# Optimization experiments

Hardware: AMD Instinct MI355X
Metric: run time of the kernel (lower is better)

The kernel has to match this reference:

```python
import jax, jax.numpy as jnp
import numpy as np
import math

EPS = 1e-5  # BatchNorm eps; eval mode with running_mean=0, running_var=1


def maxpool(x, k, p):
    return jax.lax.reduce_window(x, -jnp.inf, jax.lax.max,
                                 (1, 1, k, k), (1, 1, 1, 1),
                                 ((0, 0), (0, 0), (p, p), (p, p)))


def conv1x1(x, w, b=None):
    # x: [B,Cin,H,W], w: [Cout,Cin]
    y = jnp.einsum('oi,bihw->bohw', w, x)
    if b is not None:
        y = y + b[None, :, None, None]
    return y


def bn_eval(x, g, b):
    scale = g / jnp.sqrt(1.0 + EPS)
    return x * scale[None, :, None, None] + b[None, :, None, None]


def setup_inputs() -> dict:
    B, C, H, W = 2, 64, 80, 80
    c1, c2, c3 = 21, 21, 22
    ch = 32  # C//2
    ks = jax.random.split(jax.random.key(0), 16)
    s = 0.05
    inp = {
        'x': jax.random.normal(ks[0], (B, C, H, W), jnp.float32),
        'q1_w': jax.random.normal(ks[1], (c1, c1), jnp.float32) * s,
        'q1_g': jnp.ones((c1,), jnp.float32),
        'q1_b': jnp.zeros((c1,), jnp.float32),
        'q2_w': jax.random.normal(ks[2], (c2, c2), jnp.float32) * s,
        'q2_g': jnp.ones((c2,), jnp.float32),
        'q2_b': jnp.zeros((c2,), jnp.float32),
        'q3_w': jax.random.normal(ks[3], (c3, c3), jnp.float32) * s,
        'q3_g': jnp.ones((c3,), jnp.float32),
        'q3_b': jnp.zeros((c3,), jnp.float32),
        'k_hf_w': jax.random.normal(ks[4], (ch, C), jnp.float32) * s,
        'k_hf_b': jnp.zeros((ch,), jnp.float32),
        'k_lf_w': jax.random.normal(ks[5], (C - ch, C), jnp.float32) * s,
        'k_lf_b': jnp.zeros((C - ch,), jnp.float32),
        'k_fuse_w': jax.random.normal(ks[6], (C, C), jnp.float32) * s,
        'k_fuse_b': jnp.zeros((C,), jnp.float32),
        'v_bn_g': jnp.ones((C,), jnp.float32),
        'v_bn_b': jnp.zeros((C,), jnp.float32),
        'v_w': jax.random.normal(ks[7], (C, C), jnp.float32) * s,
        'v_b': jnp.zeros((C,), jnp.float32),
        'out_w': jax.random.normal(ks[8], (C, C), jnp.float32) * s,
        'out_b': jnp.zeros((C,), jnp.float32),
    }
    return inp


def reference(x, q1_w, q1_g, q1_b, q2_w, q2_g, q2_b, q3_w, q3_g, q3_b,
              k_hf_w, k_hf_b, k_lf_w, k_lf_b, k_fuse_w, k_fuse_b,
              v_bn_g, v_bn_b, v_w, v_b, out_w, out_b):
    B, C, H, W = x.shape
    N = H * W
    c1 = q1_w.shape[0]
    c2 = q2_w.shape[0]
    # Q: ThreeGroupConvQ (split -> 1x1 conv (no bias) -> BN -> ReLU -> concat)
    x1, x2, x3 = jnp.split(x, [c1, c1 + c2], axis=1)
    y1 = jax.nn.relu(bn_eval(conv1x1(x1, q1_w), q1_g, q1_b))
    y2 = jax.nn.relu(bn_eval(conv1x1(x2, q2_w), q2_g, q2_b))
    y3 = jax.nn.relu(bn_eval(conv1x1(x3, q3_w), q3_g, q3_b))
    Q = jnp.concatenate([y1, y2, y3], axis=1)
    # K: ThermalStructureExtractor
    p3 = maxpool(x, 3, 1)
    p5 = maxpool(x, 5, 2)
    low = (p3 + p5) * 0.5
    high = conv1x1(x - low, k_hf_w, k_hf_b)
    lowp = conv1x1(low, k_lf_w, k_lf_b)
    K = conv1x1(jnp.concatenate([high, lowp], axis=1), k_fuse_w, k_fuse_b)
    # V: BN -> 1x1 conv
    V = conv1x1(bn_eval(x, v_bn_g, v_bn_b), v_w, v_b)
    # attention over N = H*W spatial tokens, channel features
    Qc = Q.reshape(B, C, N)
    Kc = K.reshape(B, C, N)
    Vc = V.reshape(B, C, N)
    attn = jax.nn.softmax(
        jnp.einsum('bcn,bcm->bnm', Qc, Kc) / math.sqrt(C), axis=-1)  # [B,N,N]
    out = jnp.einsum('bnm,bcm->bcn', attn, Vc).reshape(B, C, H, W)
    return conv1x1(out, out_w, out_b) + x
```

## Files before the change

### kernel.cpp

```cpp
#include <hip/hip_runtime.h>
#include <hip/hip_bf16.h>


#define BATCH 2
#define CH 64
#define HH 80
#define WW 80
#define NN 6400
#define NT 100
#define KS 5
#define KTPS (NT/KS)
#define EPSV 1e-5f
#define NEGBIG (-1e30f)
#define LOG2E8 0.18033688f

typedef __hip_bfloat16 bf16;
typedef __attribute__((ext_vector_type(8))) short short8;
typedef __attribute__((ext_vector_type(4))) float f4;
#define MFMA16 __builtin_amdgcn_mfma_f32_16x16x32_bf16

__device__ __forceinline__ float b2f(bf16 v){ return __bfloat162float(v); }
__device__ __forceinline__ bf16 f2b(float v){ return __float2bfloat16(v); }
__device__ __forceinline__ ushort f2bu(float v){ return ((__hip_bfloat16_raw)__float2bfloat16(v)).x; }
__device__ __forceinline__ float bu2f(ushort u){
  union { unsigned int i; float f; } w; w.i = ((unsigned int)u) << 16; return w.f;
}
__device__ __forceinline__ unsigned pkbf(float a, float b){
  union { __hip_bfloat162 h2; unsigned u; } cv;
  cv.h2 = __float22bfloat162_rn(make_float2(a, b));
  return cv.u;
}
__device__ __forceinline__ float fexp2(float x){
#if __has_builtin(__builtin_amdgcn_exp2f)
  return __builtin_amdgcn_exp2f(x);
#else
  return exp2f(x);
#endif
}
__device__ __forceinline__ int swz(int row, int colb){
  return row*128 + (colb ^ ((row & 7) << 4));
}
__device__ __forceinline__ void sync_lds_only(){
  asm volatile("s_waitcnt lgkmcnt(0)" ::: "memory");
  __builtin_amdgcn_s_barrier();
  __builtin_amdgcn_sched_barrier(0);
  asm volatile("" ::: "memory");
}

#define OFF_BIAS 0
#define OFF_WH_B 768
#define OFF_LOW_B (768 + 32768)
#define OFF_Q_B   (OFF_LOW_B + BATCH*CH*NN*2)
#define OFF_K_B   (OFF_Q_B   + BATCH*CH*NN*2)
#define OFF_V_B   (OFF_K_B   + BATCH*CH*NN*2)
#define OFF_P_B   (OFF_V_B   + BATCH*CH*NN*2)
#define OFF_ML_B  (OFF_P_B   + BATCH*NT*KS*4096*2)

__global__ __launch_bounds__(256) void setup_fold(
    const float* __restrict__ q1w, const float* __restrict__ q1g, const float* __restrict__ q1b,
    const float* __restrict__ q2w, const float* __restrict__ q2g, const float* __restrict__ q2b,
    const float* __restrict__ q3w, const float* __restrict__ q3g, const float* __restrict__ q3b,
    const float* __restrict__ khw, const float* __restrict__ khb,
    const float* __restrict__ klw, const float* __restrict__ klb,
    const float* __restrict__ kfw, const float* __restrict__ kfb,
    const float* __restrict__ vg,  const float* __restrict__ vbnb,
    const float* __restrict__ vw,  const float* __restrict__ vb,
    const float* __restrict__ outw,
    float* __restrict__ biasf, bf16* __restrict__ wh)
{
  __shared__ __align__(16) float skf[4096];
  __shared__ __align__(16) float skh[2048];
  __shared__ __align__(16) float skl[2048];
  __shared__ __align__(16) float sow[4096];
  __shared__ __align__(16) float svw[4096];
  __shared__ float sbv[64];

  int tid = threadIdx.x;
  int blk = blockIdx.x;
  #pragma unroll
  for (int i = 0; i < 4; ++i) {
    *(float4*)&skf[(i*256 + tid)*4] = *(const float4*)&kfw[(i*256 + tid)*4];
    *(float4*)&sow[(i*256 + tid)*4] = *(const float4*)&outw[(i*256 + tid)*4];
    *(float4*)&svw[(i*256 + tid)*4] = *(const float4*)&vw[(i*256 + tid)*4];
  }
  #pragma unroll
  for (int i = 0; i < 2; ++i) {
    *(float4*)&skh[(i*256 + tid)*4] = *(const float4*)&khw[(i*256 + tid)*4];
    *(float4*)&skl[(i*256 + tid)*4] = *(const float4*)&klw[(i*256 + tid)*4];
  }
  __syncthreads();

  float rs = rsqrtf(1.0f + EPSV);
  if (tid < 64) {
    int j = tid;
    float bvo = vb[j];
    for (int ci2 = 0; ci2 < 64; ++ci2) bvo += svw[j*64 + ci2] * vbnb[ci2];
    sbv[j] = bvo;
  }

  bf16* wq   = wh;
  bf16* wvp  = wh + 4096;
  bf16* wa1  = wh + 8192;
  bf16* wa2m = wh + 12288;

  int t = blk*256 + tid;
  int ci = t & 63, co = t >> 6;
  int o = co*64 + ci;

  float w = 0.f, g;
  if (co < 21)      { g = q1g[co];    w = (ci < 21)              ? q1w[co*21 + ci]            : 0.f; }
  else if (co < 42) { g = q2g[co-21]; w = (ci >= 21 && ci < 42)  ? q2w[(co-21)*21 + (ci-21)]  : 0.f; }
  else              { g = q3g[co-42]; w = (ci >= 42)             ? q3w[(co-42)*22 + (ci-42)]  : 0.f; }
  wq[o] = f2b(w * g * rs * LOG2E8);

  float a1 = 0.f, a2 = 0.f;
  #pragma unroll
  for (int j = 0; j < 32; ++j) {
    a1 += skf[co*64 + j]      * skh[j*64 + ci];
    a2 += skf[co*64 + 32 + j] * skl[j*64 + ci];
  }
  wa1[o]  = f2b(a1);
  wa2m[o] = f2b(a2 - a1);

  float av = 0.f;
  #pragma unroll
  for (int j = 0; j < 64; ++j)
    av += sow[co*64 + j] * svw[j*64 + ci];
  wvp[o] = f2b(av * vg[ci] * rs);

  if (blk == 0 && tid < 64) {
    int c2 = tid;
    float bq;
    if (c2 < 21)      bq = q1b[c2];
    else if (c2 < 42) bq = q2b[c2-21];
    else              bq = q3b[c2-42];
    biasf[c2] = bq * LOG2E8;
    float bk = kfb[c2];
    #pragma unroll
    for (int j = 0; j < 32; ++j) {
      bk += skf[c2*64 + j]      * khb[j];
      bk += skf[c2*64 + 32 + j] * klb[j];
    }
    biasf[64 + c2] = bk;
    float bvp = 0.f;
    #pragma unroll
    for (int j = 0; j < 64; ++j) bvp += sow[c2*64 + j] * sbv[j];
    biasf[128 + c2] = bvp;
  }
}

__global__ __launch_bounds__(256) void pool_low(const float* __restrict__ x,
                                                bf16* __restrict__ lowg)
{
  int t4 = (blockIdx.x*256 + threadIdx.x)*4;
  int bc = t4 / NN; int n = t4 % NN;
  int h = n / WW, w0 = n % WW;
  const float* p = x + bc*NN;
  float m5[4], m3[4];
  #pragma unroll
  for (int j=0;j<4;++j){ m5[j]=NEGBIG; m3[j]=NEGBIG; }
  #pragma unroll
  for (int dh = -2; dh <= 2; ++dh) {
    int hh = h + dh; if (hh < 0 || hh >= HH) continue;
    float r[12];
    const float* row = p + hh*WW;
    if (w0 >= 4)      { float4 a = *(const float4*)&row[w0-4]; r[0]=a.x;r[1]=a.y;r[2]=a.z;r[3]=a.w; }
    else              { r[0]=NEGBIG;r[1]=NEGBIG;r[2]=NEGBIG;r[3]=NEGBIG; }
    { float4 a = *(const float4*)&row[w0]; r[4]=a.x;r[5]=a.y;r[6]=a.z;r[7]=a.w; }
    if (w0 + 7 < WW)  { float4 a = *(const float4*)&row[w0+4]; r[8]=a.x;r[9]=a.y;r[10]=a.z;r[11]=a.w; }
    else              { r[8]=NEGBIG;r[9]=NEGBIG;r[10]=NEGBIG;r[11]=NEGBIG; }
    bool in3 = (dh >= -1 && dh <= 1);
    #pragma unroll
    for (int j=0;j<4;++j) {
      float v3 = fmaxf(fmaxf(r[3+j], r[4+j]), r[5+j]);
      float v5 = fmaxf(fmaxf(r[2+j], v3), r[6+j]);
      m5[j] = fmaxf(m5[j], v5);
      if (in3) m3[j] = fmaxf(m3[j], v3);
    }
  }
  ushort4 o;
  o.x = f2bu(0.5f*(m3[0]+m5[0]));
  o.y = f2bu(0.5f*(m3[1]+m5[1]));
  o.z = f2bu(0.5f*(m3[2]+m5[2]));
  o.w = f2bu(0.5f*(m3[3]+m5[3]));
  *(ushort4*)&lowg[t4] = o;
}

__global__ __launch_bounds__(256, 2) void qkv_kernel(
    const float* __restrict__ x, const float* __restrict__ biasf,
    const bf16* __restrict__ wh, const bf16* __restrict__ lowg,
    bf16* __restrict__ qgT, bf16* __restrict__ kgT, bf16* __restrict__ vgc)
{
  __shared__ __align__(16) char xT[8192];
  __shared__ __align__(16) char lT[8192];
  __shared__ float bias[192];

  int tid = threadIdx.x;
  int blk = blockIdx.x;
  int b = blk / NT, tile = blk % NT;
  int n0 = tile*64;
  int wv = tid >> 6, lane = tid & 63, ln = lane & 15, quad = lane >> 4;

  if (tid < 192) bias[tid] = biasf[tid];

  {
    int cq = tid & 15, nq = tid >> 4;
    const float* xp = x + (size_t)(b*CH + cq*4)*NN + n0 + nq*4;
    float4 x0 = *(const float4*)&xp[0*NN];
    float4 x1 = *(const float4*)&xp[(size_t)1*NN];
    float4 x2 = *(const float4*)&xp[(size_t)2*NN];
    float4 x3 = *(const float4*)&xp[(size_t)3*NN];
    const bf16* lp = lowg + (size_t)(b*CH + cq*4)*NN + n0 + nq*4;
    uint2 l0 = *(const uint2*)&lp[0*NN];
    uint2 l1 = *(const uint2*)&lp[(size_t)1*NN];
    uint2 l2 = *(const uint2*)&lp[(size_t)2*NN];
    uint2 l3 = *(const uint2*)&lp[(size_t)3*NN];
    uint2 w;
    w.x = pkbf(x0.x, x1.x); w.y = pkbf(x2.x, x3.x);
    *(uint2*)(xT + swz(nq*4+0, cq*8)) = w;
    w.x = (l0.x & 0xffffu) | ((l1.x & 0xffffu) << 16);
    w.y = (l2.x & 0xffffu) | ((l3.x & 0xffffu) << 16);
    *(uint2*)(lT + swz(nq*4+0, cq*8)) = w;
    w.x = pkbf(x0.y, x1.y); w.y = pkbf(x2.y, x3.y);
    *(uint2*)(xT + swz(nq*4+1, cq*8)) = w;
    w.x = (l0.x >> 16) | ((l1.x >> 16) << 16);
    w.y = (l2.x >> 16) | ((l3.x >> 16) << 16);
    *(uint2*)(lT + swz(nq*4+1, cq*8)) = w;
    w.x = pkbf(x0.z, x1.z); w.y = pkbf(x2.z, x3.z);
    *(uint2*)(xT + swz(nq*4+2, cq*8)) = w;
    w.x = (l0.y & 0xffffu) | ((l1.y & 0xffffu) << 16);
    w.y = (l2.y & 0xffffu) | ((l3.y & 0xffffu) << 16);
    *(uint2*)(lT + swz(nq*4+2, cq*8)) = w;
    w.x = pkbf(x0.w, x1.w); w.y = pkbf(x2.w, x3.w);
    *(uint2*)(xT + swz(nq*4+3, cq*8)) = w;
    w.x = (l0.y >> 16) | ((l1.y >> 16) << 16);
    w.y = (l2.y >> 16) | ((l3.y >> 16) << 16);
    *(uint2*)(lT + swz(nq*4+3, cq*8)) = w;
  }
  __syncthreads();

  short8 xb00 = *(const short8*)(xT + swz(0*16 + ln, quad*16));
  short8 xb01 = *(const short8*)(xT + swz(0*16 + ln, 64 + quad*16));
  short8 xb10 = *(const short8*)(xT + swz(1*16 + ln, quad*16));
  short8 xb11 = *(const short8*)(xT + swz(1*16 + ln, 64 + quad*16));
  short8 xb20 = *(const short8*)(xT + swz(2*16 + ln, quad*16));
  short8 xb21 = *(const short8*)(xT + swz(2*16 + ln, 64 + quad*16));
  short8 xb30 = *(const short8*)(xT + swz(3*16 + ln, quad*16));
  short8 xb31 = *(const short8*)(xT + swz(3*16 + ln, 64 + quad*16));
  short8 xa0 = *(const short8*)(xT + swz(wv*16 + ln, quad*16));
  short8 xa1 = *(const short8*)(xT + swz(wv*16 + ln, 64 + quad*16));

  int cb = wv*16 + quad*4;
  const bf16* wqp  = wh;
  const bf16* wvpp = wh + 4096;
  const bf16* wa1p = wh + 8192;
  const bf16* wa2p = wh + 12288;
  int wrow = (wv*16 + ln)*64;

  {
    {
      short8 w0 = *(const short8*)&wvpp[(0*16 + ln)*64 + quad*8];
      short8 w1 = *(const short8*)&wvpp[(0*16 + ln)*64 + 32 + quad*8];
      float bv = bias[128 + 0*16 + ln];
      f4 a = (f4){bv, bv, bv, bv};
      a = MFMA16(xa0, w0, a, 0, 0, 0);
      a = MFMA16(xa1, w1, a, 0, 0, 0);
      uint2 pk; pk.x = pkbf(a[0], a[1]); pk.y = pkbf(a[2], a[3]);
      *(uint2*)&vgc[(size_t)(b*CH + 0*16 + ln)*NN + n0 + cb] = pk;
    }
    {
      short8 w0 = *(const short8*)&wvpp[(1*16 + ln)*64 + quad*8];
      short8 w1 = *(const short8*)&wvpp[(1*16 + ln)*64 + 32 + quad*8];
      float bv = bias[128 + 1*16 + ln];
      f4 a = (f4){bv, bv, bv, bv};
      a = MFMA16(xa0, w0, a, 0, 0, 0);
      a = MFMA16(xa1, w1, a, 0, 0, 0);
      uint2 pk; pk.x = pkbf(a[0], a[1]); pk.y = pkbf(a[2], a[3]);
      *(uint2*)&vgc[(size_t)(b*CH + 1*16 + ln)*NN + n0 + cb] = pk;
    }
    {
      short8 w0 = *(const short8*)&wvpp[(2*16 + ln)*64 + quad*8];
      short8 w1 = *(const short8*)&wvpp[(2*16 + ln)*64 + 32 + quad*8];
      float bv = bias[128 + 2*16 + ln];
      f4 a = (f4){bv, bv, bv, bv};
      a = MFMA16(xa0, w0, a, 0, 0, 0);
      a = MFMA16(xa1, w1, a, 0, 0, 0);
      uint2 pk; pk.x = pkbf(a[0], a[1]); pk.y = pkbf(a[2], a[3]);
      *(uint2*)&vgc[(size_t)(b*CH + 2*16 + ln)*NN + n0 + cb] = pk;
    }
    {
      short8 w0 = *(const short8*)&wvpp[(3*16 + ln)*64 + quad*8];
      short8 w1 = *(const short8*)&wvpp[(3*16 + ln)*64 + 32 + quad*8];
      float bv = bias[128 + 3*16 + ln];
      f4 a = (f4){bv, bv, bv, bv};
      a = MFMA16(xa0, w0, a, 0, 0, 0);
      a = MFMA16(xa1, w1, a, 0, 0, 0);
      uint2 pk; pk.x = pkbf(a[0], a[1]); pk.y = pkbf(a[2], a[3]);
      *(uint2*)&vgc[(size_t)(b*CH + 3*16 + ln)*NN + n0 + cb] = pk;
    }
  }

  {
    short8 wq0 = *(const short8*)&wqp[wrow + quad*8];
    short8 wq1 = *(const short8*)&wqp[wrow + 32 + quad*8];
    f4 bQ;
    bQ[0] = bias[cb+0]; bQ[1] = bias[cb+1]; bQ[2] = bias[cb+2]; bQ[3] = bias[cb+3];
    {
      f4 a = bQ;
      a = MFMA16(wq0, xb00, a, 0, 0, 0);
      a = MFMA16(wq1, xb01, a, 0, 0, 0);
      uint2 pk;
      pk.x = pkbf(fmaxf(a[0],0.f), fmaxf(a[1],0.f));
      pk.y = pkbf(fmaxf(a[2],0.f), fmaxf(a[3],0.f));
      *(uint2*)&qgT[(size_t)(b*NN + n0 + 0*16 + ln)*64 + cb] = pk;
    }
    {
      f4 a = bQ;
      a = MFMA16(wq0, xb10, a, 0, 0, 0);
      a = MFMA16(wq1, xb11, a, 0, 0, 0);
      uint2 pk;
      pk.x = pkbf(fmaxf(a[0],0.f), fmaxf(a[1],0.f));
      pk.y = pkbf(fmaxf(a[2],0.f), fmaxf(a[3],0.f));
      *(uint2*)&qgT[(size_t)(b*NN + n0 + 1*16 + ln)*64 + cb] = pk;
    }
    {
      f4 a = bQ;
      a = MFMA16(wq0, xb20, a, 0, 0, 0);
      a = MFMA16(wq1, xb21, a, 0, 0, 0);
      uint2 pk;
      pk.x = pkbf(fmaxf(a[0],0.f), fmaxf(a[1],0.f));
      pk.y = pkbf(fmaxf(a[2],0.f), fmaxf(a[3],0.f));
      *(uint2*)&qgT[(size_t)(b*NN + n0 + 2*16 + ln)*64 + cb] = pk;
    }
    {
      f4 a = bQ;
      a = MFMA16(wq0, xb30, a, 0, 0, 0);
      a = MFMA16(wq1, xb31, a, 0, 0, 0);
      uint2 pk;
      pk.x = pkbf(fmaxf(a[0],0.f), fmaxf(a[1],0.f));
      pk.y = pkbf(fmaxf(a[2],0.f), fmaxf(a[3],0.f));
      *(uint2*)&qgT[(size_t)(b*NN + n0 + 3*16 + ln)*64 + cb] = pk;
    }
  }

  {
    short8 wa10 = *(const short8*)&wa1p[wrow + quad*8];
    short8 wa11 = *(const short8*)&wa1p[wrow + 32 + quad*8];
    short8 wm0  = *(const short8*)&wa2p[wrow + quad*8];
    short8 wm1  = *(const short8*)&wa2p[wrow + 32 + quad*8];
    short8 lb00 = *(const short8*)(lT + swz(0*16 + ln, quad*16));
    short8 lb01 = *(const short8*)(lT + swz(0*16 + ln, 64 + quad*16));
    short8 lb10 = *(const short8*)(lT + swz(1*16 + ln, quad*16));
    short8 lb11 = *(const short8*)(lT + swz(1*16 + ln, 64 + quad*16));
    short8 lb20 = *(const short8*)(lT + swz(2*16 + ln, quad*16));
    short8 lb21 = *(const short8*)(lT + swz(2*16 + ln, 64 + quad*16));
    short8 lb30 = *(const short8*)(lT + swz(3*16 + ln, quad*16));
    short8 lb31 = *(const short8*)(lT + swz(3*16 + ln, 64 + quad*16));
    f4 bK;
    bK[0] = bias[64+cb+0]; bK[1] = bias[64+cb+1];
    bK[2] = bias[64+cb+2]; bK[3] = bias[64+cb+3];
    {
      f4 a = bK;
      a = MFMA16(wa10, xb00, a, 0, 0, 0);
      a = MFMA16(wa11, xb01, a, 0, 0, 0);
      a = MFMA16(wm0,  lb00, a, 0, 0, 0);
      a = MFMA16(wm1,  lb01, a, 0, 0, 0);
      uint2 pk; pk.x = pkbf(a[0], a[1]); pk.y = pkbf(a[2], a[3]);
      *(uint2*)&kgT[(size_t)(b*NN + n0 + 0*16 + ln)*64 + cb] = pk;
    }
    {
      f4 a = bK;
      a = MFMA16(wa10, xb10, a, 0, 0, 0);
      a = MFMA16(wa11, xb11, a, 0, 0, 0);
      a = MFMA16(wm0,  lb10, a, 0, 0, 0);
      a = MFMA16(wm1,  lb11, a, 0, 0, 0);
      uint2 pk; pk.x = pkbf(a[0], a[1]); pk.y = pkbf(a[2], a[3]);
      *(uint2*)&kgT[(size_t)(b*NN + n0 + 1*16 + ln)*64 + cb] = pk;
    }
    {
      f4 a = bK;
      a = MFMA16(wa10, xb20, a, 0, 0, 0);
      a = MFMA16(wa11, xb21, a, 0, 0, 0);
      a = MFMA16(wm0,  lb20, a, 0, 0, 0);
      a = MFMA16(wm1,  lb21, a, 0, 0, 0);
      uint2 pk; pk.x = pkbf(a[0], a[1]); pk.y = pkbf(a[2], a[3]);
      *(uint2*)&kgT[(size_t)(b*NN + n0 + 2*16 + ln)*64 + cb] = pk;
    }
    {
      f4 a = bK;
      a = MFMA16(wa10, xb30, a, 0, 0, 0);
      a = MFMA16(wa11, xb31, a, 0, 0, 0);
      a = MFMA16(wm0,  lb30, a, 0, 0, 0);
      a = MFMA16(wm1,  lb31, a, 0, 0, 0);
      uint2 pk; pk.x = pkbf(a[0], a[1]); pk.y = pkbf(a[2], a[3]);
      *(uint2*)&kgT[(size_t)(b*NN + n0 + 3*16 + ln)*64 + cb] = pk;
    }
  }
}

__global__ __launch_bounds__(256, 2) void attn_partial(
    const bf16* __restrict__ qgT, const bf16* __restrict__ kgT, const bf16* __restrict__ vgc,
    ushort* __restrict__ part, float* __restrict__ pml)
{
  __shared__ __align__(16) char smem[32768];
  __shared__ float lred[256];

  int tid = threadIdx.x;
  int blk = blockIdx.x;
  int b = blk / (NT*KS);
  int rem = blk % (NT*KS);
  int tile = rem / KS, split = rem % KS;
  int n0 = tile*64;
  int wv = tid >> 6, lane = tid & 63, ln = lane & 15, quad = lane >> 4;
  int mbase = split*KTPS*64;

  int r0 = tid >> 3,         c0 = (tid & 7)*8;
  int r1 = 32 + (tid >> 3),  c1 = (tid & 7)*8;

  {
    uint4 qa = *(const uint4*)&qgT[(size_t)(b*NN + n0 + r0)*64 + c0];
    uint4 qb = *(const uint4*)&qgT[(size_t)(b*NN + n0 + r1)*64 + c1];
    *(uint4*)(smem + swz(r0, c0*2)) = qa;
    *(uint4*)(smem + swz(r1, c1*2)) = qb;
  }
  __syncthreads();
  short8 bq00 = *(const short8*)(smem + swz( 0*16 + ln, quad*16));
  short8 bq01 = *(const short8*)(smem + swz( 0*16 + ln, 64 + quad*16));
  short8 bq10 = *(const short8*)(smem + swz( 1*16 + ln, quad*16));
  short8 bq11 = *(const short8*)(smem + swz( 1*16 + ln, 64 + quad*16));
  short8 bq20 = *(const short8*)(smem + swz( 2*16 + ln, quad*16));
  short8 bq21 = *(const short8*)(smem + swz( 2*16 + ln, 64 + quad*16));
  short8 bq30 = *(const short8*)(smem + swz( 3*16 + ln, quad*16));
  short8 bq31 = *(const short8*)(smem + swz( 3*16 + ln, 64 + quad*16));
  {
    uint4 va  = *(const uint4*)&vgc[(size_t)(b*CH + r0)*NN + mbase + c0];
    uint4 vb4 = *(const uint4*)&vgc[(size_t)(b*CH + r1)*NN + mbase + c1];
    *(uint4*)(smem + 16384 + swz(r0, c0*2)) = va;
    *(uint4*)(smem + 16384 + swz(r1, c1*2)) = vb4;
  }
  const bf16* kb = kgT + (size_t)(b*NN + mbase + wv*16 + ln)*64;
  short8 ak0 = *(const short8*)&kb[quad*8];
  short8 ak1 = *(const short8*)&kb[32 + quad*8];
  __syncthreads();

  f4 accO0 = (f4){0.f,0.f,0.f,0.f};
  f4 accO1 = (f4){0.f,0.f,0.f,0.f};
  f4 accO2 = (f4){0.f,0.f,0.f,0.f};
  f4 accO3 = (f4){0.f,0.f,0.f,0.f};
  float lacc0 = 0.f, lacc1 = 0.f, lacc2 = 0.f, lacc3 = 0.f;

  uint4 vr0, vr1;
  short8 an0, an1;
  for (int kt = 0; kt < KTPS; ++kt) {
    const int po = (kt & 1) * 8192;
    const int vo = 16384 + (kt & 1) * 8192;
    {
      int ktn = (kt + 1 < KTPS) ? kt + 1 : kt;
      int m1 = mbase + ktn*64;
      vr0 = *(const uint4*)&vgc[(size_t)(b*CH + r0)*NN + m1 + c0];
      vr1 = *(const uint4*)&vgc[(size_t)(b*CH + r1)*NN + m1 + c1];
      an0 = *(const short8*)&kb[(size_t)ktn*4096 + quad*8];
      an1 = *(const short8*)&kb[(size_t)ktn*4096 + 32 + quad*8];
    }

    f4 accS0, accS1, accS2, accS3;
    {
      f4 z = (f4){0.f,0.f,0.f,0.f};
      z = MFMA16(ak0, bq00, z, 0, 0, 0);
      accS0 = MFMA16(ak1, bq01, z, 0, 0, 0);
    }
    {
      f4 z = (f4){0.f,0.f,0.f,0.f};
      z = MFMA16(ak0, bq10, z, 0, 0, 0);
      accS1 = MFMA16(ak1, bq11, z, 0, 0, 0);
    }
    {
      f4 z = (f4){0.f,0.f,0.f,0.f};
      z = MFMA16(ak0, bq20, z, 0, 0, 0);
      accS2 = MFMA16(ak1, bq21, z, 0, 0, 0);
    }
    {
      f4 z = (f4){0.f,0.f,0.f,0.f};
      z = MFMA16(ak0, bq30, z, 0, 0, 0);
      accS3 = MFMA16(ak1, bq31, z, 0, 0, 0);
    }
    {
      float p0 = fexp2(accS0[0]), p1 = fexp2(accS0[1]);
      float p2 = fexp2(accS0[2]), p3 = fexp2(accS0[3]);
      lacc0 += (p0 + p1) + (p2 + p3);
      uint2 pk; pk.x = pkbf(p0, p1); pk.y = pkbf(p2, p3);
      *(uint2*)(smem + po + swz(0*16 + ln, wv*32 + quad*8)) = pk;
    }
    {
      float p0 = fexp2(accS1[0]), p1 = fexp2(accS1[1]);
      float p2 = fexp2(accS1[2]), p3 = fexp2(accS1[3]);
      lacc1 += (p0 + p1) + (p2 + p3);
      uint2 pk; pk.x = pkbf(p0, p1); pk.y = pkbf(p2, p3);
      *(uint2*)(smem + po + swz(1*16 + ln, wv*32 + quad*8)) = pk;
    }
    {
      float p0 = fexp2(accS2[0]), p1 = fexp2(accS2[1]);
      float p2 = fexp2(accS2[2]), p3 = fexp2(accS2[3]);
      lacc2 += (p0 + p1) + (p2 + p3);
      uint2 pk; pk.x = pkbf(p0, p1); pk.y = pkbf(p2, p3);
      *(uint2*)(smem + po + swz(2*16 + ln, wv*32 + quad*8)) = pk;
    }
    {
      float p0 = fexp2(accS3[0]), p1 = fexp2(accS3[1]);
      float p2 = fexp2(accS3[2]), p3 = fexp2(accS3[3]);
      lacc3 += (p0 + p1) + (p2 + p3);
      uint2 pk; pk.x = pkbf(p0, p1); pk.y = pkbf(p2, p3);
      *(uint2*)(smem + po + swz(3*16 + ln, wv*32 + quad*8)) = pk;
    }
    sync_lds_only();

    short8 ap0 = *(const short8*)(smem + po + swz(wv*16 + ln, quad*16));
    short8 ap1 = *(const short8*)(smem + po + swz(wv*16 + ln, 64 + quad*16));
    {
      short8 bv0 = *(const short8*)(smem + vo + swz(0*16 + ln, quad*16));
      short8 bv1 = *(const short8*)(smem + vo + swz(0*16 + ln, 64 + quad*16));
      accO0 = MFMA16(ap0, bv0, accO0, 0, 0, 0);
      accO0 = MFMA16(ap1, bv1, accO0, 0, 0, 0);
    }
    {
      short8 bv0 = *(const short8*)(smem + vo + swz(1*16 + ln, quad*16));
      short8 bv1 = *(const short8*)(smem + vo + swz(1*16 + ln, 64 + quad*16));
      accO1 = MFMA16(ap0, bv0, accO1, 0, 0, 0);
      accO1 = MFMA16(ap1, bv1, accO1, 0, 0, 0);
    }
    {
      short8 bv0 = *(const short8*)(smem + vo + swz(2*16 + ln, quad*16));
      short8 bv1 = *(const short8*)(smem + vo + swz(2*16 + ln, 64 + quad*16));
      accO2 = MFMA16(ap0, bv0, accO2, 0, 0, 0);
      accO2 = MFMA16(ap1, bv1, accO2, 0, 0, 0);
    }
    {
      short8 bv0 = *(const short8*)(smem + vo + swz(3*16 + ln, quad*16));
      short8 bv1 = *(const short8*)(smem + vo + swz(3*16 + ln, 64 + quad*16));
      accO3 = MFMA16(ap0, bv0, accO3, 0, 0, 0);
      accO3 = MFMA16(ap1, bv1, accO3, 0, 0, 0);
    }
    if (kt + 1 < KTPS) {
      int vn = 16384 + ((kt+1) & 1) * 8192;
      *(uint4*)(smem + vn + swz(r0, c0*2)) = vr0;
      *(uint4*)(smem + vn + swz(r1, c1*2)) = vr1;
    }
    ak0 = an0; ak1 = an1;
  }

  size_t pbase = ((size_t)(b*NT + tile)*KS + split)*4096;
  ushort* pp = part + pbase;
  {
    uint2 pk; pk.x = pkbf(accO0[0], accO0[1]); pk.y = pkbf(accO0[2], accO0[3]);
    *(uint2*)&pp[(0*16 + ln)*64 + wv*16 + quad*4] = pk;
  }
  {
    uint2 pk; pk.x = pkbf(accO1[0], accO1[1]); pk.y = pkbf(accO1[2], accO1[3]);
    *(uint2*)&pp[(1*16 + ln)*64 + wv*16 + quad*4] = pk;
  }
  {
    uint2 pk; pk.x = pkbf(accO2[0], accO2[1]); pk.y = pkbf(accO2[2], accO2[3]);
    *(uint2*)&pp[(2*16 + ln)*64 + wv*16 + quad*4] = pk;
  }
  {
    uint2 pk; pk.x = pkbf(accO3[0], accO3[1]); pk.y = pkbf(accO3[2], accO3[3]);
    *(uint2*)&pp[(3*16 + ln)*64 + wv*16 + quad*4] = pk;
  }
  {
    float s = lacc0;
    s += __shfl_xor(s, 16); s += __shfl_xor(s, 32);
    if (quad == 0) lred[wv*64 + 0*16 + ln] = s;
  }
  {
    float s = lacc1;
    s += __shfl_xor(s, 16); s += __shfl_xor(s, 32);
    if (quad == 0) lred[wv*64 + 1*16 + ln] = s;
  }
  {
    float s = lacc2;
    s += __shfl_xor(s, 16); s += __shfl_xor(s, 32);
    if (quad == 0) lred[wv*64 + 2*16 + ln] = s;
  }
  {
    float s = lacc3;
    s += __shfl_xor(s, 16); s += __shfl_xor(s, 32);
    if (quad == 0) lred[wv*64 + 3*16 + ln] = s;
  }
  __syncthreads();
  if (tid < 64) {
    size_t mlb = ((size_t)(b*NT + tile)*KS + split)*64;
    pml[mlb + tid] = (lred[tid] + lred[64 + tid]) + (lred[128 + tid] + lred[192 + tid]);
  }
}

__global__ __launch_bounds__(256) void attn_reduce(
    const ushort* __restrict__ part, const float* __restrict__ pml,
    const float* __restrict__ x, const float* __restrict__ outb,
    float* __restrict__ out)
{
  __shared__ float linv[64];
  __shared__ float ob[64];

  int tid = threadIdx.x;
  int blk = blockIdx.x;
  int b = blk / NT, tile = blk % NT;
  size_t base = (size_t)(b*NT + tile)*KS;

  if (tid < 64) {
    float l = 0.f;
    #pragma unroll
    for (int s=0;s<KS;++s) l += pml[(base+s)*64 + tid];
    linv[tid] = 1.0f / l;
    ob[tid] = outb[tid];
  }
  __syncthreads();

  #pragma unroll
  for (int j = 0; j < 4; ++j) {
    int idx = j*256 + tid;
    int c = idx >> 4, q = idx & 15;
    float a0=0.f, a1=0.f, a2=0.f, a3=0.f;
    #pragma unroll
    for (int s = 0; s < KS; ++s) {
      uint2 v = *(const uint2*)&part[(base+s)*4096 + (size_t)c*64 + q*4];
      a0 += bu2f((ushort)(v.x & 0xffff)); a1 += bu2f((ushort)(v.x >> 16));
      a2 += bu2f((ushort)(v.y & 0xffff)); a3 += bu2f((ushort)(v.y >> 16));
    }
    int nl = q*4;
    size_t gidx = (size_t)(b*CH + c)*NN + tile*64 + nl;
    float4 xv = *(const float4*)&x[gidx];
    float bc = ob[c];
    float4 o;
    o.x = a0*linv[nl+0] + bc + xv.x;
    o.y = a1*linv[nl+1] + bc + xv.y;
    o.z = a2*linv[nl+2] + bc + xv.z;
    o.w = a3*linv[nl+3] + bc + xv.w;
    *(float4*)&out[gidx] = o;
  }
}

extern "C" void kernel_launch(void* const* d_in, const int* in_sizes, int n_in,
                              void* d_out, int out_size, void* d_ws, size_t ws_size,
                              hipStream_t stream) {
  const float* x    = (const float*)d_in[0];
  const float* q1w  = (const float*)d_in[1];
  const float* q1g  = (const float*)d_in[2];
  const float* q1b  = (const float*)d_in[3];
  const float* q2w  = (const float*)d_in[4];
  const float* q2g  = (const float*)d_in[5];
  const float* q2b  = (const float*)d_in[6];
  const float* q3w  = (const float*)d_in[7];
  const float* q3g  = (const float*)d_in[8];
  const float* q3b  = (const float*)d_in[9];
  const float* khw  = (const float*)d_in[10];
  const float* khb  = (const float*)d_in[11];
  const float* klw  = (const float*)d_in[12];
  const float* klb  = (const float*)d_in[13];
  const float* kfw  = (const float*)d_in[14];
  const float* kfb  = (const float*)d_in[15];
  const float* vbg  = (const float*)d_in[16];
  const float* vbb  = (const float*)d_in[17];
  const float* vw   = (const float*)d_in[18];
  const float* vb   = (const float*)d_in[19];
  const float* outw = (const float*)d_in[20];
  const float* outb = (const float*)d_in[21];

  char*   wsb  = (char*)d_ws;
  float*  biasf= (float*)(wsb + OFF_BIAS);
  bf16*   wh   = (bf16*)(wsb + OFF_WH_B);
  bf16*   lowg = (bf16*)(wsb + OFF_LOW_B);
  bf16*   qgT  = (bf16*)(wsb + OFF_Q_B);
  bf16*   kgT  = (bf16*)(wsb + OFF_K_B);
  bf16*   vgc  = (bf16*)(wsb + OFF_V_B);
  ushort* part = (ushort*)(wsb + OFF_P_B);
  float*  pml  = (float*)(wsb + OFF_ML_B);

  hipLaunchKernelGGL(setup_fold, dim3(16), dim3(256), 0, stream,
                     q1w,q1g,q1b,q2w,q2g,q2b,q3w,q3g,q3b,
                     khw,khb,klw,klb,kfw,kfb,vbg,vbb,vw,vb,outw, biasf, wh);
  hipLaunchKernelGGL(pool_low, dim3(BATCH*CH*NN/1024), dim3(256), 0, stream, x, lowg);
  hipLaunchKernelGGL(qkv_kernel, dim3(BATCH*NT), dim3(256), 0, stream,
                     x, biasf, wh, lowg, qgT, kgT, vgc);
  hipLaunchKernelGGL(attn_partial, dim3(BATCH*NT*KS), dim3(256), 0, stream,
                     qgT, kgT, vgc, part, pml);
  hipLaunchKernelGGL(attn_reduce, dim3(BATCH*NT), dim3(256), 0, stream,
                     part, pml, x, outb, (float*)d_out);
}
```

Measured before the change: 148.2 us.

## Retile PV MFMA into 2x2 warp grid and raise MFMA wave priority

The P·V step changes from each wave owning 16 query rows across all 64 channels to a 2x2 split: each wave takes 32 query rows and 32 channels. Each wave now loads 4 P fragments and 4 V fragments from LDS instead of 2 P and 8 V. This lowers the LDS read traffic per MFMA. The output write indices are remapped to match. s_setprio brackets are also placed around the MFMA groups to favour issue of matrix work across waves, at the cost of more live registers for the fragments.

Result: no change. 148.7 us (+0.3%).

```diff
diff --git a/kernel.cpp b/kernel.cpp
--- a/kernel.cpp
+++ b/kernel.cpp
@@ -412,6 +412,7 @@
   int tile = rem / KS, split = rem % KS;
   int n0 = tile*64;
   int wv = tid >> 6, lane = tid & 63, ln = lane & 15, quad = lane >> 4;
+  int cw = wv >> 1, nw = wv & 1;
   int mbase = split*KTPS*64;
 
   int r0 = tid >> 3,         c0 = (tid & 7)*8;
@@ -464,6 +465,7 @@
     }
 
     f4 accS0, accS1, accS2, accS3;
+    __builtin_amdgcn_s_setprio(1);
     {
       f4 z = (f4){0.f,0.f,0.f,0.f};
       z = MFMA16(ak0, bq00, z, 0, 0, 0);
@@ -484,6 +486,7 @@
       z = MFMA16(ak0, bq30, z, 0, 0, 0);
       accS3 = MFMA16(ak1, bq31, z, 0, 0, 0);
     }
+    __builtin_amdgcn_s_setprio(0);
     {
       float p0 = fexp2(accS0[0]), p1 = fexp2(accS0[1]);
       float p2 = fexp2(accS0[2]), p3 = fexp2(accS0[3]);
@@ -514,32 +517,24 @@
     }
     sync_lds_only();
 
-    short8 ap0 = *(const short8*)(smem + po + swz(wv*16 + ln, quad*16));
-    short8 ap1 = *(const short8*)(smem + po + swz(wv*16 + ln, 64 + quad*16));
-    {
-      short8 bv0 = *(const short8*)(smem + vo + swz(0*16 + ln, quad*16));
-      short8 bv1 = *(const short8*)(smem + vo + swz(0*16 + ln, 64 + quad*16));
-      accO0 = MFMA16(ap0, bv0, accO0, 0, 0, 0);
-      accO0 = MFMA16(ap1, bv1, accO0, 0, 0, 0);
-    }
-    {
-      short8 bv0 = *(const short8*)(smem + vo + swz(1*16 + ln, quad*16));
-      short8 bv1 = *(const short8*)(smem + vo + swz(1*16 + ln, 64 + quad*16));
-      accO1 = MFMA16(ap0, bv0, accO1, 0, 0, 0);
-      accO1 = MFMA16(ap1, bv1, accO1, 0, 0, 0);
-    }
-    {
-      short8 bv0 = *(const short8*)(smem + vo + swz(2*16 + ln, quad*16));
-      short8 bv1 = *(const short8*)(smem + vo + swz(2*16 + ln, 64 + quad*16));
-      accO2 = MFMA16(ap0, bv0, accO2, 0, 0, 0);
-      accO2 = MFMA16(ap1, bv1, accO2, 0, 0, 0);
-    }
-    {
-      short8 bv0 = *(const short8*)(smem + vo + swz(3*16 + ln, quad*16));
-      short8 bv1 = *(const short8*)(smem + vo + swz(3*16 + ln, 64 + quad*16));
-      accO3 = MFMA16(ap0, bv0, accO3, 0, 0, 0);
-      accO3 = MFMA16(ap1, bv1, accO3, 0, 0, 0);
-    }
+    short8 ap00 = *(const short8*)(smem + po + swz(nw*32 + 0*16 + ln, quad*16));
+    short8 ap01 = *(const short8*)(smem + po + swz(nw*32 + 0*16 + ln, 64 + quad*16));
+    short8 ap10 = *(const short8*)(smem + po + swz(nw*32 + 1*16 + ln, quad*16));
+    short8 ap11 = *(const short8*)(smem + po + swz(nw*32 + 1*16 + ln, 64 + quad*16));
+    short8 bv00 = *(const short8*)(smem + vo + swz(cw*32 + 0*16 + ln, quad*16));
+    short8 bv01 = *(const short8*)(smem + vo + swz(cw*32 + 0*16 + ln, 64 + quad*16));
+    short8 bv10 = *(const short8*)(smem + vo + swz(cw*32 + 1*16 + ln, quad*16));
+    short8 bv11 = *(const short8*)(smem + vo + swz(cw*32 + 1*16 + ln, 64 + quad*16));
+    __builtin_amdgcn_s_setprio(1);
+    accO0 = MFMA16(ap00, bv00, accO0, 0, 0, 0);
+    accO0 = MFMA16(ap01, bv01, accO0, 0, 0, 0);
+    accO1 = MFMA16(ap00, bv10, accO1, 0, 0, 0);
+    accO1 = MFMA16(ap01, bv11, accO1, 0, 0, 0);
+    accO2 = MFMA16(ap10, bv00, accO2, 0, 0, 0);
+    accO2 = MFMA16(ap11, bv01, accO2, 0, 0, 0);
+    accO3 = MFMA16(ap10, bv10, accO3, 0, 0, 0);
+    accO3 = MFMA16(ap11, bv11, accO3, 0, 0, 0);
+    __builtin_amdgcn_s_setprio(0);
     if (kt + 1 < KTPS) {
       int vn = 16384 + ((kt+1) & 1) * 8192;
       *(uint4*)(smem + vn + swz(r0, c0*2)) = vr0;
@@ -552,19 +547,19 @@
   ushort* pp = part + pbase;
   {
     uint2 pk; pk.x = pkbf(accO0[0], accO0[1]); pk.y = pkbf(accO0[2], accO0[3]);
-    *(uint2*)&pp[(0*16 + ln)*64 + wv*16 + quad*4] = pk;
+    *(uint2*)&pp[(cw*32 + 0*16 + ln)*64 + nw*32 + 0*16 + quad*4] = pk;
   }
   {
     uint2 pk; pk.x = pkbf(accO1[0], accO1[1]); pk.y = pkbf(accO1[2], accO1[3]);
-    *(uint2*)&pp[(1*16 + ln)*64 + wv*16 + quad*4] = pk;
+    *(uint2*)&pp[(cw*32 + 1*16 + ln)*64 + nw*32 + 0*16 + quad*4] = pk;
   }
   {
     uint2 pk; pk.x = pkbf(accO2[0], accO2[1]); pk.y = pkbf(accO2[2], accO2[3]);
-    *(uint2*)&pp[(2*16 + ln)*64 + wv*16 + quad*4] = pk;
+    *(uint2*)&pp[(cw*32 + 0*16 + ln)*64 + nw*32 + 1*16 + quad*4] = pk;
   }
   {
     uint2 pk; pk.x = pkbf(accO3[0], accO3[1]); pk.y = pkbf(accO3[2], accO3[3]);
-    *(uint2*)&pp[(3*16 + ln)*64 + wv*16 + quad*4] = pk;
+    *(uint2*)&pp[(cw*32 + 1*16 + ln)*64 + nw*32 + 1*16 + quad*4] = pk;
   }
   {
     float s = lacc0;
```
